# Performance work log

Hardware: AMD Instinct MI355X
Metric: run time of the kernel (lower is better)

Reference implementation:

```python
import jax, jax.numpy as jnp
import numpy as np

B, C, H, W = 8, 320, 64, 64      # query feature map
S_KV, D_KV = 77, 1024            # key/value (text) tokens
HEADS, DIM_HEAD = 8, 64
INNER = HEADS * DIM_HEAD         # 512


def setup_inputs() -> dict:
    key = jax.random.key(0)
    ks = jax.random.split(key, 7)
    return {
        "query": jax.random.normal(ks[0], (B, C, H, W), dtype=jnp.float32),
        "key_value": jax.random.normal(ks[1], (B, S_KV, D_KV), dtype=jnp.float32),
        "Wq": jax.random.normal(ks[2], (C, INNER), dtype=jnp.float32) * (C ** -0.5),
        "Wk": jax.random.normal(ks[3], (D_KV, INNER), dtype=jnp.float32) * (D_KV ** -0.5),
        "Wv": jax.random.normal(ks[4], (D_KV, INNER), dtype=jnp.float32) * (D_KV ** -0.5),
        "Wo": jax.random.normal(ks[5], (INNER, C), dtype=jnp.float32) * (INNER ** -0.5),
        "bo": jnp.zeros((C,), dtype=jnp.float32),
    }


def reference(query, key_value, Wq, Wk, Wv, Wo, bo):
    b, c, h, w = query.shape
    n = h * w
    # [B,C,H,W] -> [B,N,C]
    q_flat = query.reshape(b, c, n).transpose(0, 2, 1)
    # projections, then split heads: [B, S, heads, dim_head]
    q = (q_flat @ Wq).reshape(b, n, HEADS, DIM_HEAD)
    k = (key_value @ Wk).reshape(b, S_KV, HEADS, DIM_HEAD)
    v = (key_value @ Wv).reshape(b, S_KV, HEADS, DIM_HEAD)
    scale = DIM_HEAD ** -0.5
    # attn logits: [B, heads, N, S_kv]
    logits = jnp.einsum('bnhd,bshd->bhns', q, k) * scale
    attn = jax.nn.softmax(logits, axis=-1)
    # weighted values -> merge heads: [B, N, inner]
    out = jnp.einsum('bhns,bshd->bnhd', attn, v).reshape(b, n, INNER)
    out = out @ Wo + bo  # dropout p=0.0 is identity
    # [B,N,C] -> [B,C,H,W]
    return out.transpose(0, 2, 1).reshape(b, c, h, w)
```

## Files before the change

### kernel.cpp

```cpp
#include <hip/hip_runtime.h>
#include <hip/hip_bf16.h>
#include <stdint.h>

#define BB     8
#define CC     320
#define NN     4096
#define SKV    77
#define HEADS  8
#define INNER  512
#define SCALE  0.125f

typedef float f32x4  __attribute__((ext_vector_type(4)));
typedef short bf16x8 __attribute__((ext_vector_type(8)));
typedef short s16x4  __attribute__((ext_vector_type(4)));

static __device__ __forceinline__ short f2bf(float f) {
  unsigned u = __float_as_uint(f);
  return (short)((u + 0x7fffu + ((u >> 16) & 1u)) >> 16);
}

static __device__ __forceinline__ void gll16(void* lds, const void* g) {
  auto gp = reinterpret_cast<const uint32_t __attribute__((address_space(1)))*>(
      reinterpret_cast<uintptr_t>(g));
  auto lp = reinterpret_cast<uint32_t __attribute__((address_space(3)))*>(
      reinterpret_cast<uintptr_t>(lds));
  __builtin_amdgcn_global_load_lds(gp, lp, 16, 0, 0);
}

__global__ __launch_bounds__(256) void prep_kernel(
    const float* __restrict__ kv, const float* __restrict__ Wk,
    const float* __restrict__ Wv, const float* __restrict__ Wq,
    const float* __restrict__ Wo, short* __restrict__ kv_bf,
    short* __restrict__ Wk_t, short* __restrict__ Wv_t,
    short* __restrict__ Wq_t, short* __restrict__ Wo_t,
    unsigned* __restrict__ zero_base) {
  __shared__ float T[64 * 65];
  const int blk = blockIdx.x, t = threadIdx.x;
  if (blk < 616) {
    const int base = blk * 1024;
    #pragma unroll
    for (int i = 0; i < 4; ++i) kv_bf[base + i*256 + t] = f2bf(kv[base + i*256 + t]);
    return;
  }
  if (blk >= 952) {
    const int base = (blk - 952) * 1024;
    #pragma unroll
    for (int i = 0; i < 4; ++i) zero_base[base + i*256 + t] = 0u;
    return;
  }
  const float* src; short* dst; int RS, CS, kt, ct;
  if (blk < 872) {
    const int tile = blk - 616;
    const bool isK = tile < 128;
    const int tt = isK ? tile : tile - 128;
    src = isK ? Wk : Wv; dst = isK ? Wk_t : Wv_t;
    RS = 1024; CS = 512; kt = tt >> 3; ct = tt & 7;
  } else if (blk < 912) {
    const int tt = blk - 872;
    src = Wq; dst = Wq_t; RS = 320; CS = 512; kt = tt >> 3; ct = tt & 7;
  } else {
    const int tt = blk - 912;
    src = Wo; dst = Wo_t; RS = 512; CS = 320; kt = tt / 5; ct = tt % 5;
  }
  const int cl = t & 63, rb = t >> 6;
  #pragma unroll
  for (int i = 0; i < 16; ++i)
    T[(rb + i*4)*65 + cl] = src[(size_t)(kt*64 + rb + i*4)*CS + ct*64 + cl];
  __syncthreads();
  #pragma unroll
  for (int i = 0; i < 16; ++i) {
    const int nl = rb + i*4;
    dst[(size_t)(ct*64 + nl)*RS + kt*64 + cl] = f2bf(T[cl*65 + nl]);
  }
}

__global__ __launch_bounds__(256) void xpose_kernel(
    const float* __restrict__ query, short* __restrict__ X_bf) {
  __shared__ float T[64 * 65];
  const int bx = blockIdx.x, t = threadIdx.x;
  const int b = bx / 320, r = bx % 320;
  const int nt = r / 5, ct = r % 5;
  const int tl = t & 63, rb = t >> 6;
  #pragma unroll
  for (int i = 0; i < 16; ++i) {
    const int c = rb + i*4;
    T[c*65 + tl] = query[((size_t)(b*CC + ct*64 + c))*NN + nt*64 + tl];
  }
  __syncthreads();
  #pragma unroll
  for (int i = 0; i < 16; ++i) {
    const int n = rb + i*4;
    X_bf[((size_t)(b*NN + nt*64 + n))*CC + ct*64 + tl] = f2bf(T[tl*65 + n]);
  }
}

__global__ __launch_bounds__(256) void kvproj_kernel(
    const short* __restrict__ kv_bf, const short* __restrict__ Wk_t,
    const short* __restrict__ Wv_t, short* __restrict__ K_ws,
    short* __restrict__ V_ws) {
  const int t = threadIdx.x, w = t >> 6, lane = t & 63;
  const int l15 = lane & 15, q = lane >> 4;
  const int m0 = (blockIdx.x * 4 + w) * 16;
  const int y = blockIdx.y;
  const bool isK = (y < 8);
  const int h = y & 7;
  const short* __restrict__ Wt = isK ? Wk_t : Wv_t;
  const int arow = (m0 + l15 < 616) ? (m0 + l15) : 615;

  const f32x4 z = {0.f, 0.f, 0.f, 0.f};
  f32x4 acc[4] = {z, z, z, z};
  for (int k0 = 0; k0 < 1024; k0 += 32) {
    const bf16x8 a = *(const bf16x8*)(kv_bf + arow*1024 + k0 + q*8);
    #pragma unroll
    for (int nt = 0; nt < 4; ++nt) {
      const int n = h*64 + nt*16 + l15;
      const bf16x8 bfr = *(const bf16x8*)(Wt + n*1024 + k0 + q*8);
      acc[nt] = __builtin_amdgcn_mfma_f32_16x16x32_bf16(a, bfr, acc[nt], 0, 0, 0);
    }
  }
  #pragma unroll
  for (int nt = 0; nt < 4; ++nt) {
    const int d = nt*16 + l15;
    #pragma unroll
    for (int r = 0; r < 4; ++r) {
      const int row = m0 + q*4 + r;
      if (row < 616) {
        const int b = (int)(((unsigned)row * 54472u) >> 22);
        const int s = row - b*77;
        if (isK) K_ws[((b*8 + h)*80 + s)*64 + d] = f2bf(acc[nt][r]);
        else     V_ws[((b*8 + h)*64 + d)*96 + s] = f2bf(acc[nt][r]);
      }
    }
  }
}

__global__ __launch_bounds__(256) void qproj_kernel(
    const short* __restrict__ X_bf, const short* __restrict__ Wq_t,
    short* __restrict__ Q_ws) {
  const int t = threadIdx.x, w = t >> 6, lane = t & 63;
  const int l15 = lane & 15, q = lane >> 4;
  const int m0 = (blockIdx.x >> 2) * 128;
  const int n0 = (blockIdx.x & 3) * 128;
  const int wm = w & 1, wn = w >> 1;

  __shared__ short tile[8192];

  const f32x4 z = {0.f, 0.f, 0.f, 0.f};
  f32x4 acc[4][4];
  #pragma unroll
  for (int mt = 0; mt < 4; ++mt)
    #pragma unroll
    for (int nt = 0; nt < 4; ++nt) acc[mt][nt] = z;

  for (int it = 0; it < 10; ++it) {
    const int k0 = it * 32;
    if (it) __syncthreads();
    #pragma unroll
    for (int p = 0; p < 2; ++p) {
      const int f = p*256 + t, row = f >> 2, c4 = f & 3;
      gll16(tile + f*8, X_bf + (size_t)(m0 + row)*320 + k0 + c4*8);
    }
    #pragma unroll
    for (int p = 0; p < 2; ++p) {
      const int f = p*256 + t, row = f >> 2, c4 = f & 3;
      gll16(tile + 4096 + f*8, Wq_t + (size_t)(n0 + row)*320 + k0 + c4*8);
    }
    __syncthreads();
    bf16x8 a[4], bb[4];
    #pragma unroll
    for (int mt = 0; mt < 4; ++mt)
      a[mt] = *(const bf16x8*)(tile + (wm*64 + mt*16 + l15)*32 + q*8);
    #pragma unroll
    for (int nt = 0; nt < 4; ++nt)
      bb[nt] = *(const bf16x8*)(tile + 4096 + (wn*64 + nt*16 + l15)*32 + q*8);
    #pragma unroll
    for (int mt = 0; mt < 4; ++mt)
      #pragma unroll
      for (int nt = 0; nt < 4; ++nt)
        acc[mt][nt] = __builtin_amdgcn_mfma_f32_16x16x32_bf16(a[mt], bb[nt], acc[mt][nt], 0, 0, 0);
  }
  #pragma unroll
  for (int mt = 0; mt < 4; ++mt)
    #pragma unroll
    for (int r = 0; r < 4; ++r) {
      short* rowp = Q_ws + (size_t)(m0 + wm*64 + mt*16 + q*4 + r)*512 + n0 + wn*64;
      #pragma unroll
      for (int nt = 0; nt < 4; ++nt)
        rowp[nt*16 + l15] = f2bf(acc[mt][nt][r]);
    }
}

__global__ __launch_bounds__(64) void attncore_kernel(
    const short* __restrict__ Q_ws, const short* __restrict__ K_ws,
    const short* __restrict__ V_ws, short* __restrict__ O_ws) {
  const int bx = blockIdx.x;
  const int h = bx & 7;
  const int g = bx >> 3;
  const int b = g >> 7;
  const int n0 = (g & 127) * 32;
  const int lane = threadIdx.x;
  const int l15 = lane & 15, q = lane >> 4;

  __shared__ short scr[32 * 104];
  for (int i = lane; i < 32*104/2; i += 64) ((unsigned*)scr)[i] = 0u;

  const short* __restrict__ Kh = K_ws + (size_t)(b*8 + h) * 80 * 64;
  const short* __restrict__ Vh = V_ws + (size_t)(b*8 + h) * 64 * 96;
  size_t tokrow[2];
  #pragma unroll
  for (int nt = 0; nt < 2; ++nt) tokrow[nt] = (size_t)(b*NN + n0 + nt*16 + l15);

  const f32x4 z = {0.f, 0.f, 0.f, 0.f};
  f32x4 qk[2][5];
  #pragma unroll
  for (int nt = 0; nt < 2; ++nt)
    #pragma unroll
    for (int st = 0; st < 5; ++st) qk[nt][st] = z;
  #pragma unroll
  for (int f = 0; f < 2; ++f) {
    bf16x8 bq[2];
    #pragma unroll
    for (int nt = 0; nt < 2; ++nt)
      bq[nt] = *(const bf16x8*)(Q_ws + tokrow[nt]*512 + h*64 + f*32 + q*8);
    #pragma unroll
    for (int st = 0; st < 5; ++st) {
      const bf16x8 a = *(const bf16x8*)(Kh + (st*16 + l15)*64 + f*32 + q*8);
      #pragma unroll
      for (int nt = 0; nt < 2; ++nt)
        qk[nt][st] = __builtin_amdgcn_mfma_f32_16x16x32_bf16(a, bq[nt], qk[nt][st], 0, 0, 0);
    }
  }

  #pragma unroll
  for (int nt = 0; nt < 2; ++nt) {
    float mx = -1e30f;
    #pragma unroll
    for (int st = 0; st < 5; ++st)
      #pragma unroll
      for (int r = 0; r < 4; ++r) {
        const int s = st*16 + q*4 + r;
        const float vv = (s < SKV) ? qk[nt][st][r] * SCALE : -1e30f;
        qk[nt][st][r] = vv;
        mx = fmaxf(mx, vv);
      }
    mx = fmaxf(mx, __shfl_xor(mx, 16));
    mx = fmaxf(mx, __shfl_xor(mx, 32));
    float sum = 0.f;
    #pragma unroll
    for (int st = 0; st < 5; ++st)
      #pragma unroll
      for (int r = 0; r < 4; ++r) {
        const int s = st*16 + q*4 + r;
        const float e = (s < SKV) ? __expf(qk[nt][st][r] - mx) : 0.f;
        qk[nt][st][r] = e;
        sum += e;
      }
    sum += __shfl_xor(sum, 16);
    sum += __shfl_xor(sum, 32);
    const float inv = 1.0f / sum;
    #pragma unroll
    for (int st = 0; st < 5; ++st) {
      s16x4 pv;
      #pragma unroll
      for (int r = 0; r < 4; ++r) pv[r] = f2bf(qk[nt][st][r] * inv);
      *(s16x4*)(scr + (nt*16 + l15)*104 + st*16 + q*4) = pv;
    }
  }

  f32x4 ov[2][4];
  #pragma unroll
  for (int nt = 0; nt < 2; ++nt)
    #pragma unroll
    for (int dt = 0; dt < 4; ++dt) ov[nt][dt] = z;
  #pragma unroll
  for (int f = 0; f < 3; ++f) {
    bf16x8 bp[2];
    #pragma unroll
    for (int nt = 0; nt < 2; ++nt)
      bp[nt] = *(const bf16x8*)(scr + (nt*16 + l15)*104 + f*32 + q*8);
    #pragma unroll
    for (int dt = 0; dt < 4; ++dt) {
      const bf16x8 a = *(const bf16x8*)(Vh + (dt*16 + l15)*96 + f*32 + q*8);
      #pragma unroll
      for (int nt = 0; nt < 2; ++nt)
        ov[nt][dt] = __builtin_amdgcn_mfma_f32_16x16x32_bf16(a, bp[nt], ov[nt][dt], 0, 0, 0);
    }
  }
  #pragma unroll
  for (int nt = 0; nt < 2; ++nt)
    #pragma unroll
    for (int dt = 0; dt < 4; ++dt) {
      s16x4 pv;
      #pragma unroll
      for (int r = 0; r < 4; ++r) pv[r] = f2bf(ov[nt][dt][r]);
      *(s16x4*)(O_ws + tokrow[nt]*512 + h*64 + dt*16 + q*4) = pv;
    }
}

__global__ __launch_bounds__(256) void outproj_kernel(
    const short* __restrict__ O_ws, const short* __restrict__ Wo_t,
    const float* __restrict__ bo, float* __restrict__ out) {
  const int t = threadIdx.x, w = t >> 6, lane = t & 63;
  const int l15 = lane & 15, q = lane >> 4;
  const int c0 = (blockIdx.x & 1) * 160;
  const int t0 = (blockIdx.x >> 1) * 128;
  const int wm = w & 1, wn = w >> 1;

  __shared__ short tile[9216];

  const f32x4 z = {0.f, 0.f, 0.f, 0.f};
  f32x4 acc[5][4];
  #pragma unroll
  for (int mt = 0; mt < 5; ++mt)
    #pragma unroll
    for (int nt = 0; nt < 4; ++nt) acc[mt][nt] = z;

  for (int it = 0; it < 16; ++it) {
    const int k0 = it * 32;
    if (it) __syncthreads();
    #pragma unroll
    for (int p = 0; p < 5; ++p) {
      const int f = p*256 + t;
      if (f < 1152) {
        const short* g;
        if (f < 640) {
          const int row = f >> 2, c4 = f & 3;
          g = Wo_t + (size_t)(c0 + row)*512 + k0 + c4*8;
        } else {
          const int f2 = f - 640, row = f2 >> 2, c4 = f2 & 3;
          g = O_ws + (size_t)(t0 + row)*512 + k0 + c4*8;
        }
        gll16(tile + f*8, g);
      }
    }
    __syncthreads();
    bf16x8 a[5], bb[4];
    #pragma unroll
    for (int mt = 0; mt < 5; ++mt)
      a[mt] = *(const bf16x8*)(tile + (wm*80 + mt*16 + l15)*32 + q*8);
    #pragma unroll
    for (int nt = 0; nt < 4; ++nt)
      bb[nt] = *(const bf16x8*)(tile + 5120 + (wn*64 + nt*16 + l15)*32 + q*8);
    #pragma unroll
    for (int mt = 0; mt < 5; ++mt)
      #pragma unroll
      for (int nt = 0; nt < 4; ++nt)
        acc[mt][nt] = __builtin_amdgcn_mfma_f32_16x16x32_bf16(a[mt], bb[nt], acc[mt][nt], 0, 0, 0);
  }
  const int b = t0 >> 12, n = t0 & 4095;
  #pragma unroll
  for (int mt = 0; mt < 5; ++mt)
    #pragma unroll
    for (int r = 0; r < 4; ++r) {
      const int c = c0 + wm*80 + mt*16 + q*4 + r;
      const float bv = bo[c];
      float* rowp = out + ((size_t)(b*CC + c))*NN + n + wn*64;
      #pragma unroll
      for (int nt = 0; nt < 4; ++nt)
        rowp[nt*16 + l15] = acc[mt][nt][r] + bv;
    }
}

extern "C" void kernel_launch(void* const* d_in, const int* in_sizes, int n_in,
                              void* d_out, int out_size, void* d_ws, size_t ws_size,
                              hipStream_t stream) {
  const float* query = (const float*)d_in[0];
  const float* kv    = (const float*)d_in[1];
  const float* Wq    = (const float*)d_in[2];
  const float* Wk    = (const float*)d_in[3];
  const float* Wv    = (const float*)d_in[4];
  const float* Wo    = (const float*)d_in[5];
  const float* bo    = (const float*)d_in[6];
  float* out = (float*)d_out;

  char* p = (char*)d_ws;
  short* K_ws  = (short*)(p);
  short* V_ws  = (short*)(p +   819200);
  short* Wq_t  = (short*)(p +  1802240);
  short* Wo_t  = (short*)(p +  2129920);
  short* Q_ws  = (short*)(p +  2457600);
  char* pb = p + 36012032;
  short* X_bf  = (short*)(pb);
  short* kv_bf = (short*)(pb + 20971520);
  short* Wk_t  = (short*)(pb + 22233088);
  short* Wv_t  = (short*)(pb + 23281664);
  short* O_ws  = (short*)(pb);

  prep_kernel<<<1392, 256, 0, stream>>>(kv, Wk, Wv, Wq, Wo, kv_bf, Wk_t, Wv_t,
                                        Wq_t, Wo_t, (unsigned*)p);
  xpose_kernel<<<2560, 256, 0, stream>>>(query, X_bf);
  kvproj_kernel<<<dim3(10, 16), 256, 0, stream>>>(kv_bf, Wk_t, Wv_t, K_ws, V_ws);
  qproj_kernel<<<1024, 256, 0, stream>>>(X_bf, Wq_t, Q_ws);
  attncore_kernel<<<8192, 64, 0, stream>>>(Q_ws, K_ws, V_ws, O_ws);
  outproj_kernel<<<512, 256, 0, stream>>>(O_ws, Wo_t, bo, out);
}
```

Baseline: 197.2 us.

## Merge query transpose into prep kernel, fold scale into Wq, widen qproj and attncore blocks

Moves the query transpose/bf16 conversion into the prep kernel as extra blocks, dropping one launch. Folds the softmax scale into the transposed Wq so attention no longer multiplies logits by it. Widens the Q projection tile to 128x256 per block with 2-wave occupancy hints, and packs four attention units per 256-thread block, each wave using its own LDS scratch. Larger register and LDS footprint may cut occupancy, and scaling Wq before bf16 rounding changes rounding slightly.

```diff
diff --git a/kernel.cpp b/kernel.cpp
--- a/kernel.cpp
+++ b/kernel.cpp
@@ -30,9 +30,10 @@
 __global__ __launch_bounds__(256) void prep_kernel(
     const float* __restrict__ kv, const float* __restrict__ Wk,
     const float* __restrict__ Wv, const float* __restrict__ Wq,
-    const float* __restrict__ Wo, short* __restrict__ kv_bf,
-    short* __restrict__ Wk_t, short* __restrict__ Wv_t,
-    short* __restrict__ Wq_t, short* __restrict__ Wo_t,
+    const float* __restrict__ Wo, const float* __restrict__ query,
+    short* __restrict__ kv_bf, short* __restrict__ Wk_t,
+    short* __restrict__ Wv_t, short* __restrict__ Wq_t,
+    short* __restrict__ Wo_t, short* __restrict__ X_bf,
     unsigned* __restrict__ zero_base) {
   __shared__ float T[64 * 65];
   const int blk = blockIdx.x, t = threadIdx.x;
@@ -42,13 +43,31 @@
     for (int i = 0; i < 4; ++i) kv_bf[base + i*256 + t] = f2bf(kv[base + i*256 + t]);
     return;
   }
+  if (blk >= 1392) {
+    const int blk2 = blk - 1392;
+    const int b = blk2 / 320, r = blk2 % 320;
+    const int nt = r / 5, ct = r % 5;
+    const int tl = t & 63, rb = t >> 6;
+    #pragma unroll
+    for (int i = 0; i < 16; ++i) {
+      const int c = rb + i*4;
+      T[c*65 + tl] = query[((size_t)(b*CC + ct*64 + c))*NN + nt*64 + tl];
+    }
+    __syncthreads();
+    #pragma unroll
+    for (int i = 0; i < 16; ++i) {
+      const int n = rb + i*4;
+      X_bf[((size_t)(b*NN + nt*64 + n))*CC + ct*64 + tl] = f2bf(T[tl*65 + n]);
+    }
+    return;
+  }
   if (blk >= 952) {
     const int base = (blk - 952) * 1024;
     #pragma unroll
     for (int i = 0; i < 4; ++i) zero_base[base + i*256 + t] = 0u;
     return;
   }
-  const float* src; short* dst; int RS, CS, kt, ct;
+  const float* src; short* dst; int RS, CS, kt, ct; float scl = 1.0f;
   if (blk < 872) {
     const int tile = blk - 616;
     const bool isK = tile < 128;
@@ -58,6 +77,7 @@
   } else if (blk < 912) {
     const int tt = blk - 872;
     src = Wq; dst = Wq_t; RS = 320; CS = 512; kt = tt >> 3; ct = tt & 7;
+    scl = SCALE;
   } else {
     const int tt = blk - 912;
     src = Wo; dst = Wo_t; RS = 512; CS = 320; kt = tt / 5; ct = tt % 5;
@@ -70,27 +90,7 @@
   #pragma unroll
   for (int i = 0; i < 16; ++i) {
     const int nl = rb + i*4;
-    dst[(size_t)(ct*64 + nl)*RS + kt*64 + cl] = f2bf(T[cl*65 + nl]);
-  }
-}
-
-__global__ __launch_bounds__(256) void xpose_kernel(
-    const float* __restrict__ query, short* __restrict__ X_bf) {
-  __shared__ float T[64 * 65];
-  const int bx = blockIdx.x, t = threadIdx.x;
-  const int b = bx / 320, r = bx % 320;
-  const int nt = r / 5, ct = r % 5;
-  const int tl = t & 63, rb = t >> 6;
-  #pragma unroll
-  for (int i = 0; i < 16; ++i) {
-    const int c = rb + i*4;
-    T[c*65 + tl] = query[((size_t)(b*CC + ct*64 + c))*NN + nt*64 + tl];
-  }
-  __syncthreads();
-  #pragma unroll
-  for (int i = 0; i < 16; ++i) {
-    const int n = rb + i*4;
-    X_bf[((size_t)(b*NN + nt*64 + n))*CC + ct*64 + tl] = f2bf(T[tl*65 + n]);
+    dst[(size_t)(ct*64 + nl)*RS + kt*64 + cl] = f2bf(T[cl*65 + nl] * scl);
   }
 }
 
@@ -134,23 +134,23 @@
   }
 }
 
-__global__ __launch_bounds__(256) void qproj_kernel(
+__global__ __launch_bounds__(256, 2) void qproj_kernel(
     const short* __restrict__ X_bf, const short* __restrict__ Wq_t,
     short* __restrict__ Q_ws) {
   const int t = threadIdx.x, w = t >> 6, lane = t & 63;
   const int l15 = lane & 15, q = lane >> 4;
-  const int m0 = (blockIdx.x >> 2) * 128;
-  const int n0 = (blockIdx.x & 3) * 128;
+  const int m0 = (blockIdx.x >> 1) * 128;
+  const int n0 = (blockIdx.x & 1) * 256;
   const int wm = w & 1, wn = w >> 1;
 
-  __shared__ short tile[8192];
+  __shared__ short tile[12288];
 
   const f32x4 z = {0.f, 0.f, 0.f, 0.f};
-  f32x4 acc[4][4];
+  f32x4 acc[4][8];
   #pragma unroll
   for (int mt = 0; mt < 4; ++mt)
     #pragma unroll
-    for (int nt = 0; nt < 4; ++nt) acc[mt][nt] = z;
+    for (int nt = 0; nt < 8; ++nt) acc[mt][nt] = z;
 
   for (int it = 0; it < 10; ++it) {
     const int k0 = it * 32;
@@ -161,48 +161,49 @@
       gll16(tile + f*8, X_bf + (size_t)(m0 + row)*320 + k0 + c4*8);
     }
     #pragma unroll
-    for (int p = 0; p < 2; ++p) {
+    for (int p = 0; p < 4; ++p) {
       const int f = p*256 + t, row = f >> 2, c4 = f & 3;
       gll16(tile + 4096 + f*8, Wq_t + (size_t)(n0 + row)*320 + k0 + c4*8);
     }
     __syncthreads();
-    bf16x8 a[4], bb[4];
+    bf16x8 a[4], bb[8];
     #pragma unroll
     for (int mt = 0; mt < 4; ++mt)
       a[mt] = *(const bf16x8*)(tile + (wm*64 + mt*16 + l15)*32 + q*8);
     #pragma unroll
-    for (int nt = 0; nt < 4; ++nt)
-      bb[nt] = *(const bf16x8*)(tile + 4096 + (wn*64 + nt*16 + l15)*32 + q*8);
+    for (int nt = 0; nt < 8; ++nt)
+      bb[nt] = *(const bf16x8*)(tile + 4096 + (wn*128 + nt*16 + l15)*32 + q*8);
     #pragma unroll
     for (int mt = 0; mt < 4; ++mt)
       #pragma unroll
-      for (int nt = 0; nt < 4; ++nt)
+      for (int nt = 0; nt < 8; ++nt)
         acc[mt][nt] = __builtin_amdgcn_mfma_f32_16x16x32_bf16(a[mt], bb[nt], acc[mt][nt], 0, 0, 0);
   }
   #pragma unroll
   for (int mt = 0; mt < 4; ++mt)
     #pragma unroll
     for (int r = 0; r < 4; ++r) {
-      short* rowp = Q_ws + (size_t)(m0 + wm*64 + mt*16 + q*4 + r)*512 + n0 + wn*64;
-      #pragma unroll
-      for (int nt = 0; nt < 4; ++nt)
+      short* rowp = Q_ws + (size_t)(m0 + wm*64 + mt*16 + q*4 + r)*512 + n0 + wn*128;
+      #pragma unroll
+      for (int nt = 0; nt < 8; ++nt)
         rowp[nt*16 + l15] = f2bf(acc[mt][nt][r]);
     }
 }
 
-__global__ __launch_bounds__(64) void attncore_kernel(
+__global__ __launch_bounds__(256) void attncore_kernel(
     const short* __restrict__ Q_ws, const short* __restrict__ K_ws,
     const short* __restrict__ V_ws, short* __restrict__ O_ws) {
-  const int bx = blockIdx.x;
-  const int h = bx & 7;
-  const int g = bx >> 3;
+  const int t = threadIdx.x, w = t >> 6, lane = t & 63;
+  const int unit = blockIdx.x * 4 + w;
+  const int h = unit & 7;
+  const int g = unit >> 3;
   const int b = g >> 7;
   const int n0 = (g & 127) * 32;
-  const int lane = threadIdx.x;
   const int l15 = lane & 15, q = lane >> 4;
 
-  __shared__ short scr[32 * 104];
-  for (int i = lane; i < 32*104/2; i += 64) ((unsigned*)scr)[i] = 0u;
+  __shared__ short scr[4 * 32 * 104];
+  short* scrw = scr + w * 32 * 104;
+  for (int i = lane; i < 32*104/2; i += 64) ((unsigned*)scrw)[i] = 0u;
 
   const short* __restrict__ Kh = K_ws + (size_t)(b*8 + h) * 80 * 64;
   const short* __restrict__ Vh = V_ws + (size_t)(b*8 + h) * 64 * 96;
@@ -239,7 +240,7 @@
       #pragma unroll
       for (int r = 0; r < 4; ++r) {
         const int s = st*16 + q*4 + r;
-        const float vv = (s < SKV) ? qk[nt][st][r] * SCALE : -1e30f;
+        const float vv = (s < SKV) ? qk[nt][st][r] : -1e30f;
         qk[nt][st][r] = vv;
         mx = fmaxf(mx, vv);
       }
@@ -263,7 +264,7 @@
       s16x4 pv;
       #pragma unroll
       for (int r = 0; r < 4; ++r) pv[r] = f2bf(qk[nt][st][r] * inv);
-      *(s16x4*)(scr + (nt*16 + l15)*104 + st*16 + q*4) = pv;
+      *(s16x4*)(scrw + (nt*16 + l15)*104 + st*16 + q*4) = pv;
     }
   }
 
@@ -277,7 +278,7 @@
     bf16x8 bp[2];
     #pragma unroll
     for (int nt = 0; nt < 2; ++nt)
-      bp[nt] = *(const bf16x8*)(scr + (nt*16 + l15)*104 + f*32 + q*8);
+      bp[nt] = *(const bf16x8*)(scrw + (nt*16 + l15)*104 + f*32 + q*8);
     #pragma unroll
     for (int dt = 0; dt < 4; ++dt) {
       const bf16x8 a = *(const bf16x8*)(Vh + (dt*16 + l15)*96 + f*32 + q*8);
@@ -386,11 +387,11 @@
   short* Wv_t  = (short*)(pb + 23281664);
   short* O_ws  = (short*)(pb);
 
-  prep_kernel<<<1392, 256, 0, stream>>>(kv, Wk, Wv, Wq, Wo, kv_bf, Wk_t, Wv_t,
-                                        Wq_t, Wo_t, (unsigned*)p);
-  xpose_kernel<<<2560, 256, 0, stream>>>(query, X_bf);
+  prep_kernel<<<3952, 256, 0, stream>>>(kv, Wk, Wv, Wq, Wo, query, kv_bf,
+                                        Wk_t, Wv_t, Wq_t, Wo_t, X_bf,
+                                        (unsigned*)p);
   kvproj_kernel<<<dim3(10, 16), 256, 0, stream>>>(kv_bf, Wk_t, Wv_t, K_ws, V_ws);
-  qproj_kernel<<<1024, 256, 0, stream>>>(X_bf, Wq_t, Q_ws);
-  attncore_kernel<<<8192, 64, 0, stream>>>(Q_ws, K_ws, V_ws, O_ws);
+  qproj_kernel<<<512, 256, 0, stream>>>(X_bf, Wq_t, Q_ws);
+  attncore_kernel<<<2048, 256, 0, stream>>>(Q_ws, K_ws, V_ws, O_ws);
   outproj_kernel<<<512, 256, 0, stream>>>(O_ws, Wo_t, bo, out);
 }
```

New measurement: 192.0 us. 2.6% less time.
